# Performance work log

Measured on AMD Instinct MI355X. Metric: run time of the kernel, lower is better.

The kernel has to match this reference:

```python
import jax, jax.numpy as jnp
import numpy as np

MIN_EXPERTS = 1
MAX_EXPERTS = 8
TEMPERATURE = 1.0


def setup_inputs() -> dict:
    key = jax.random.key(0)
    ks = jax.random.split(key, 7)
    B, S, H, E = 8, 4096, 1024, 64
    Hh = H // 2
    return {
        "hidden_states": jax.random.normal(ks[0], (B, S, H), dtype=jnp.float32),
        "W_router": jax.random.normal(ks[1], (E, H), dtype=jnp.float32) * 0.02,
        "b_router": jax.random.normal(ks[2], (E,), dtype=jnp.float32) * 0.02,
        "W1": jax.random.normal(ks[3], (Hh, H), dtype=jnp.float32) * 0.02,
        "b1": jax.random.normal(ks[4], (Hh,), dtype=jnp.float32) * 0.02,
        "W2": jax.random.normal(ks[5], (1, Hh), dtype=jnp.float32) * 0.02,
        "b2": jax.random.normal(ks[6], (1,), dtype=jnp.float32) * 0.02,
    }


def reference(hidden_states, W_router, b_router, W1, b1, W2, b2):
    B, S, H = hidden_states.shape
    flat = hidden_states.reshape(-1, H)                     # [N, H]

    # router logits
    router_logits = (flat @ W_router.T + b_router) / TEMPERATURE  # [N, E]

    # confidence net: Linear -> ReLU -> Linear -> Sigmoid
    h = jax.nn.relu(flat @ W1.T + b1)                       # [N, H/2]
    confidence = jax.nn.sigmoid(h @ W2.T + b2).squeeze(-1)  # [N]

    # dynamic k per token (torch.round = half-to-even, same as jnp.round)
    dk = MIN_EXPERTS + (MAX_EXPERTS - MIN_EXPERTS) * (1.0 - confidence)
    dk = jnp.clip(jnp.round(dk), MIN_EXPERTS, MAX_EXPERTS).astype(jnp.int32)  # [N]

    routing_probs = jax.nn.softmax(router_logits, axis=-1)  # [N, E]

    # single top-k pass replaces per-iteration sort; mask slots >= dynamic_k
    top_vals, top_idx = jax.lax.top_k(routing_probs, MAX_EXPERTS)  # [N, max_k]
    slot = jnp.arange(MAX_EXPERTS, dtype=jnp.int32)[None, :]       # [1, max_k]
    active = slot < dk[:, None]                                    # [N, max_k]
    sel_w = jnp.where(active, top_vals, 0.0)
    sel_i = jnp.where(active, top_idx, 0).astype(jnp.int64)

    sel_w = sel_w.reshape(B, S, MAX_EXPERTS)
    sel_i = sel_i.reshape(B, S, MAX_EXPERTS)
    return sel_w, sel_i, confidence, router_logits
```

## Files before the change

### kernel.cpp

```cpp
#include <hip/hip_runtime.h>
#include <hip/hip_bf16.h>
#include <math.h>

#define N_TOK 32768
#define HDIM 1024
#define HH 512
#define NOUT 576
#define BM 256
#define BN 64
#define BK 32
#define THREADS 256
#define KC 384

#define OFF_SELW 0
#define OFF_SELI 262144
#define OFF_CONF 524288
#define OFF_LOG  557056

__device__ float  g_Bmat[HDIM * NOUT];
__device__ double g_partial[N_TOK * 8];

__global__ __launch_bounds__(256) void k_build(const float* __restrict__ W1,
                                               const float* __restrict__ Wr) {
  int idx = blockIdx.x * 256 + threadIdx.x;
  int k = idx / NOUT;
  int j = idx - k * NOUT;
  float v = (j < HH) ? W1[(size_t)j * HDIM + k] : Wr[(size_t)(j - HH) * HDIM + k];
  g_Bmat[idx] = v;
}

__global__ __launch_bounds__(THREADS, 2) void k_gemm(const float* __restrict__ A,
                                                     const float* __restrict__ b1,
                                                     const float* __restrict__ W2,
                                                     const float* __restrict__ b_router,
                                                     float* __restrict__ out_logits) {
  __shared__ float As[BK][BM];
  __shared__ float Bs[BK][BN];

  int bid = blockIdx.x;
  int xcd = bid & 7;
  int s   = bid >> 3;
  int j   = s % 9;
  int t   = xcd + 8 * (s / 9);

  const int tid = threadIdx.x;
  const int tx  = tid & 7;
  const int ty  = tid >> 3;
  const int m0  = t * BM;
  const int n0  = j * BN;

  float acc[8][8];
  float carry[8][8];
  #pragma unroll
  for (int i = 0; i < 8; ++i)
    #pragma unroll
    for (int c = 0; c < 8; ++c) { acc[i][c] = 0.f; carry[i][c] = 0.f; }

  const float* Ag = A + (size_t)(m0 + tid) * HDIM;

  for (int k0 = 0; k0 < HDIM; k0 += BK) {
    if (k0 == KC || k0 == 2 * KC) {
      #pragma unroll
      for (int i = 0; i < 8; ++i)
        #pragma unroll
        for (int c = 0; c < 8; ++c) {
          carry[i][c] = carry[i][c] + acc[i][c];
          acc[i][c] = 0.f;
        }
    }

    float4 av[8];
    #pragma unroll
    for (int c = 0; c < 8; ++c)
      av[c] = *(const float4*)(Ag + k0 + c * 4);
    float4 bv[2];
    #pragma unroll
    for (int c = 0; c < 2; ++c) {
      int idx = tid + c * 256;
      int kr  = idx >> 4;
      int ch  = idx & 15;
      bv[c] = *(const float4*)&g_Bmat[(size_t)(k0 + kr) * NOUT + n0 + ch * 4];
    }
    __syncthreads();
    #pragma unroll
    for (int c = 0; c < 8; ++c) {
      int kb = c * 4;
      As[kb + 0][tid] = av[c].x;
      As[kb + 1][tid] = av[c].y;
      As[kb + 2][tid] = av[c].z;
      As[kb + 3][tid] = av[c].w;
    }
    #pragma unroll
    for (int c = 0; c < 2; ++c) {
      int idx = tid + c * 256;
      int kr  = idx >> 4;
      int ch  = idx & 15;
      *(float4*)&Bs[kr][ch * 4] = bv[c];
    }
    __syncthreads();

    #pragma unroll 4
    for (int kk = 0; kk < BK; ++kk) {
      float4 a03 = *(const float4*)&As[kk][ty * 8 + 0];
      float4 a47 = *(const float4*)&As[kk][ty * 8 + 4];
      float4 b03 = *(const float4*)&Bs[kk][tx * 8 + 0];
      float4 b47 = *(const float4*)&Bs[kk][tx * 8 + 4];
      float a[8] = {a03.x, a03.y, a03.z, a03.w, a47.x, a47.y, a47.z, a47.w};
      float b[8] = {b03.x, b03.y, b03.z, b03.w, b47.x, b47.y, b47.z, b47.w};
      #pragma unroll
      for (int i = 0; i < 8; ++i)
        #pragma unroll
        for (int c = 0; c < 8; ++c)
          acc[i][c] = fmaf(a[i], b[c], acc[i][c]);
    }
  }

  #pragma unroll
  for (int i = 0; i < 8; ++i)
    #pragma unroll
    for (int c = 0; c < 8; ++c) carry[i][c] = carry[i][c] + acc[i][c];

  if (j < 8) {
    double w2v[8];
    float  b1v[8];
    #pragma unroll
    for (int c = 0; c < 8; ++c) {
      w2v[c] = (double)W2[n0 + tx * 8 + c];
      b1v[c] = b1[n0 + tx * 8 + c];
    }
    #pragma unroll
    for (int i = 0; i < 8; ++i) {
      double sacc = 0.0;
      #pragma unroll
      for (int c = 0; c < 8; ++c) {
        float h = fmaxf(carry[i][c] + b1v[c], 0.f);
        sacc = fma((double)h, w2v[c], sacc);
      }
      sacc += __shfl_xor(sacc, 1, 64);
      sacc += __shfl_xor(sacc, 2, 64);
      sacc += __shfl_xor(sacc, 4, 64);
      if (tx == 0) g_partial[(size_t)(m0 + ty * 8 + i) * 8 + j] = sacc;
    }
  } else {
    float brv[8];
    #pragma unroll
    for (int c = 0; c < 8; ++c) brv[c] = b_router[tx * 8 + c];
    #pragma unroll
    for (int i = 0; i < 8; ++i) {
      int row = m0 + ty * 8 + i;
      float o[8];
      #pragma unroll
      for (int c = 0; c < 8; ++c) o[c] = carry[i][c] + brv[c];
      float* dst = out_logits + (size_t)row * 64 + tx * 8;
      *(float4*)dst       = make_float4(o[0], o[1], o[2], o[3]);
      *(float4*)(dst + 4) = make_float4(o[4], o[5], o[6], o[7]);
    }
  }
}

__global__ __launch_bounds__(256, 2) void k_post(const float* __restrict__ b2,
                                                 float* __restrict__ d_out) {
  int tk = blockIdx.x * 256 + threadIdx.x;

  double ca = (double)b2[0];
  #pragma unroll
  for (int jj = 0; jj < 8; ++jj) ca += g_partial[(size_t)tk * 8 + jj];
  double conf = 1.0 / (1.0 + exp(-ca));
  double dkf  = 1.0 + 7.0 * (1.0 - conf);
  double dkr  = rint(dkf);
  int dk = (int)fmin(fmax(dkr, 1.0), 8.0);

  const float* logits = d_out + OFF_LOG + (size_t)tk * 64;
  float x[64];
  #pragma unroll
  for (int e4 = 0; e4 < 16; ++e4)
    *(float4*)&x[e4 * 4] = *(const float4*)&logits[e4 * 4];

  float mx = x[0];
  #pragma unroll
  for (int e = 1; e < 64; ++e) mx = fmaxf(mx, x[e]);

  #pragma unroll
  for (int e = 0; e < 64; ++e) x[e] = expf(x[e] - mx);

  float r[8];
  #pragma unroll
  for (int q = 0; q < 8; ++q) r[q] = x[q];
  #pragma unroll
  for (int b = 1; b < 8; ++b)
    #pragma unroll
    for (int q = 0; q < 8; ++q) r[q] += x[b * 8 + q];
  float ssum = ((r[0] + r[1]) + (r[2] + r[3])) + ((r[4] + r[5]) + (r[6] + r[7]));

  #pragma unroll
  for (int e = 0; e < 64; ++e) x[e] = x[e] / ssum;

  float* sel_w = d_out + OFF_SELW + (size_t)tk * 8;
  float* sel_i = d_out + OFF_SELI + (size_t)tk * 8;
  unsigned long long used = 0ull;
  #pragma unroll
  for (int slot = 0; slot < 8; ++slot) {
    float best = -1.f;
    int   bi   = 0;
    #pragma unroll
    for (int e = 0; e < 64; ++e) {
      bool ok = (((used >> e) & 1ull) == 0ull) && (x[e] > best);
      best = ok ? x[e] : best;
      bi   = ok ? e    : bi;
    }
    used |= (1ull << bi);
    bool active = slot < dk;
    sel_w[slot] = active ? best : 0.f;
    sel_i[slot] = active ? (float)bi : 0.f;
  }
  d_out[OFF_CONF + tk] = (float)conf;
}

extern "C" void kernel_launch(void* const* d_in, const int* in_sizes, int n_in,
                              void* d_out, int out_size, void* d_ws, size_t ws_size,
                              hipStream_t stream) {
  const float* hidden   = (const float*)d_in[0];
  const float* W_router = (const float*)d_in[1];
  const float* b_router = (const float*)d_in[2];
  const float* W1       = (const float*)d_in[3];
  const float* b1       = (const float*)d_in[4];
  const float* W2       = (const float*)d_in[5];
  const float* b2       = (const float*)d_in[6];
  float* out = (float*)d_out;

  k_build<<<(HDIM * NOUT) / 256, 256, 0, stream>>>(W1, W_router);
  k_gemm<<<(N_TOK / BM) * 9, THREADS, 0, stream>>>(hidden, b1, W2, b_router,
                                                   out + OFF_LOG);
  k_post<<<N_TOK / 256, 256, 0, stream>>>(b2, out);
}
```

Before: 699.0 us.

## Replace LDS-tiled GEMM with per-thread row dot products over 16-column tiles

The shared-memory tiled 8x8 register-blocked GEMM is replaced by a scheme where each thread owns one token row and computes 16 output columns. A comes straight from global memory as float4, and B rows are uniform across the wave, so they become broadcast/scalar loads. This removes the LDS staging and barriers and raises occupancy. In exchange, each thread issues uncoalesced strided loads of its own A row, and A is re-read 36 times instead of 9. The confidence partial sums grow from 8 to 32 per token.

```diff
diff --git a/kernel.cpp b/kernel.cpp
--- a/kernel.cpp
+++ b/kernel.cpp
@@ -6,19 +6,17 @@
 #define HDIM 1024
 #define HH 512
 #define NOUT 576
-#define BM 256
-#define BN 64
-#define BK 32
+#define CT 16
+#define NCT 36
 #define THREADS 256
-#define KC 384
 
 #define OFF_SELW 0
 #define OFF_SELI 262144
 #define OFF_CONF 524288
 #define OFF_LOG  557056
 
-__device__ float  g_Bmat[HDIM * NOUT];
-__device__ double g_partial[N_TOK * 8];
+__device__ __attribute__((aligned(256))) float g_Bmat[HDIM * NOUT];
+__device__ double g_partial[N_TOK * 32];
 
 __global__ __launch_bounds__(256) void k_build(const float* __restrict__ W1,
                                                const float* __restrict__ Wr) {
@@ -29,132 +27,64 @@
   g_Bmat[idx] = v;
 }
 
-__global__ __launch_bounds__(THREADS, 2) void k_gemm(const float* __restrict__ A,
+__global__ __launch_bounds__(THREADS, 8) void k_gemm(const float* __restrict__ A,
                                                      const float* __restrict__ b1,
                                                      const float* __restrict__ W2,
                                                      const float* __restrict__ b_router,
                                                      float* __restrict__ out_logits) {
-  __shared__ float As[BK][BM];
-  __shared__ float Bs[BK][BN];
-
   int bid = blockIdx.x;
   int xcd = bid & 7;
   int s   = bid >> 3;
-  int j   = s % 9;
-  int t   = xcd + 8 * (s / 9);
+  int ct  = s % NCT;
+  int tg  = xcd + 8 * (s / NCT);
 
-  const int tid = threadIdx.x;
-  const int tx  = tid & 7;
-  const int ty  = tid >> 3;
-  const int m0  = t * BM;
-  const int n0  = j * BN;
+  const int m  = tg * 256 + threadIdx.x;
+  const int j0 = ct * CT;
 
-  float acc[8][8];
-  float carry[8][8];
+  const float* __restrict__ Ag = A + (size_t)m * HDIM;
+  const float* __restrict__ Bg = g_Bmat + j0;
+
+  float acc[CT], carry[CT];
   #pragma unroll
-  for (int i = 0; i < 8; ++i)
-    #pragma unroll
-    for (int c = 0; c < 8; ++c) { acc[i][c] = 0.f; carry[i][c] = 0.f; }
+  for (int c = 0; c < CT; ++c) { acc[c] = 0.f; carry[c] = 0.f; }
 
-  const float* Ag = A + (size_t)(m0 + tid) * HDIM;
-
-  for (int k0 = 0; k0 < HDIM; k0 += BK) {
-    if (k0 == KC || k0 == 2 * KC) {
+  const int kb[4] = {0, 384, 768, 1024};
+  #pragma unroll
+  for (int p = 0; p < 3; ++p) {
+    for (int k0 = kb[p]; k0 < kb[p + 1]; k0 += 4) {
+      float4 av = *(const float4*)(Ag + k0);
+      const float a4[4] = {av.x, av.y, av.z, av.w};
       #pragma unroll
-      for (int i = 0; i < 8; ++i)
+      for (int kk = 0; kk < 4; ++kk) {
+        const float* __restrict__ brow = Bg + (size_t)(k0 + kk) * NOUT;
+        float a = a4[kk];
         #pragma unroll
-        for (int c = 0; c < 8; ++c) {
-          carry[i][c] = carry[i][c] + acc[i][c];
-          acc[i][c] = 0.f;
-        }
-    }
-
-    float4 av[8];
-    #pragma unroll
-    for (int c = 0; c < 8; ++c)
-      av[c] = *(const float4*)(Ag + k0 + c * 4);
-    float4 bv[2];
-    #pragma unroll
-    for (int c = 0; c < 2; ++c) {
-      int idx = tid + c * 256;
-      int kr  = idx >> 4;
-      int ch  = idx & 15;
-      bv[c] = *(const float4*)&g_Bmat[(size_t)(k0 + kr) * NOUT + n0 + ch * 4];
-    }
-    __syncthreads();
-    #pragma unroll
-    for (int c = 0; c < 8; ++c) {
-      int kb = c * 4;
-      As[kb + 0][tid] = av[c].x;
-      As[kb + 1][tid] = av[c].y;
-      As[kb + 2][tid] = av[c].z;
-      As[kb + 3][tid] = av[c].w;
+        for (int c = 0; c < CT; ++c)
+          acc[c] = fmaf(a, brow[c], acc[c]);
+      }
     }
     #pragma unroll
-    for (int c = 0; c < 2; ++c) {
-      int idx = tid + c * 256;
-      int kr  = idx >> 4;
-      int ch  = idx & 15;
-      *(float4*)&Bs[kr][ch * 4] = bv[c];
-    }
-    __syncthreads();
-
-    #pragma unroll 4
-    for (int kk = 0; kk < BK; ++kk) {
-      float4 a03 = *(const float4*)&As[kk][ty * 8 + 0];
-      float4 a47 = *(const float4*)&As[kk][ty * 8 + 4];
-      float4 b03 = *(const float4*)&Bs[kk][tx * 8 + 0];
-      float4 b47 = *(const float4*)&Bs[kk][tx * 8 + 4];
-      float a[8] = {a03.x, a03.y, a03.z, a03.w, a47.x, a47.y, a47.z, a47.w};
-      float b[8] = {b03.x, b03.y, b03.z, b03.w, b47.x, b47.y, b47.z, b47.w};
-      #pragma unroll
-      for (int i = 0; i < 8; ++i)
-        #pragma unroll
-        for (int c = 0; c < 8; ++c)
-          acc[i][c] = fmaf(a[i], b[c], acc[i][c]);
-    }
+    for (int c = 0; c < CT; ++c) { carry[c] = carry[c] + acc[c]; acc[c] = 0.f; }
   }
 
-  #pragma unroll
-  for (int i = 0; i < 8; ++i)
+  if (ct < 32) {
+    double sacc = 0.0;
     #pragma unroll
-    for (int c = 0; c < 8; ++c) carry[i][c] = carry[i][c] + acc[i][c];
-
-  if (j < 8) {
-    double w2v[8];
-    float  b1v[8];
+    for (int c = 0; c < CT; ++c) {
+      float h = fmaxf(carry[c] + b1[j0 + c], 0.f);
+      sacc = fma((double)h, (double)W2[j0 + c], sacc);
+    }
+    g_partial[(size_t)m * 32 + ct] = sacc;
+  } else {
+    int jr = (ct - 32) * CT;
+    float o[CT];
     #pragma unroll
-    for (int c = 0; c < 8; ++c) {
-      w2v[c] = (double)W2[n0 + tx * 8 + c];
-      b1v[c] = b1[n0 + tx * 8 + c];
-    }
+    for (int c = 0; c < CT; ++c) o[c] = carry[c] + b_router[jr + c];
+    float* dst = out_logits + (size_t)m * 64 + jr;
     #pragma unroll
-    for (int i = 0; i < 8; ++i) {
-      double sacc = 0.0;
-      #pragma unroll
-      for (int c = 0; c < 8; ++c) {
-        float h = fmaxf(carry[i][c] + b1v[c], 0.f);
-        sacc = fma((double)h, w2v[c], sacc);
-      }
-      sacc += __shfl_xor(sacc, 1, 64);
-      sacc += __shfl_xor(sacc, 2, 64);
-      sacc += __shfl_xor(sacc, 4, 64);
-      if (tx == 0) g_partial[(size_t)(m0 + ty * 8 + i) * 8 + j] = sacc;
-    }
-  } else {
-    float brv[8];
-    #pragma unroll
-    for (int c = 0; c < 8; ++c) brv[c] = b_router[tx * 8 + c];
-    #pragma unroll
-    for (int i = 0; i < 8; ++i) {
-      int row = m0 + ty * 8 + i;
-      float o[8];
-      #pragma unroll
-      for (int c = 0; c < 8; ++c) o[c] = carry[i][c] + brv[c];
-      float* dst = out_logits + (size_t)row * 64 + tx * 8;
-      *(float4*)dst       = make_float4(o[0], o[1], o[2], o[3]);
-      *(float4*)(dst + 4) = make_float4(o[4], o[5], o[6], o[7]);
-    }
+    for (int c4 = 0; c4 < 4; ++c4)
+      *(float4*)(dst + c4 * 4) =
+          make_float4(o[c4 * 4], o[c4 * 4 + 1], o[c4 * 4 + 2], o[c4 * 4 + 3]);
   }
 }
 
@@ -164,7 +94,7 @@
 
   double ca = (double)b2[0];
   #pragma unroll
-  for (int jj = 0; jj < 8; ++jj) ca += g_partial[(size_t)tk * 8 + jj];
+  for (int jj = 0; jj < 32; ++jj) ca += g_partial[(size_t)tk * 32 + jj];
   double conf = 1.0 / (1.0 + exp(-ca));
   double dkf  = 1.0 + 7.0 * (1.0 - conf);
   double dkr  = rint(dkf);
@@ -229,7 +159,7 @@
   float* out = (float*)d_out;
 
   k_build<<<(HDIM * NOUT) / 256, 256, 0, stream>>>(W1, W_router);
-  k_gemm<<<(N_TOK / BM) * 9, THREADS, 0, stream>>>(hidden, b1, W2, b_router,
-                                                   out + OFF_LOG);
+  k_gemm<<<(N_TOK / 256) * NCT, THREADS, 0, stream>>>(hidden, b1, W2, b_router,
+                                                      out + OFF_LOG);
   k_post<<<N_TOK / 256, 256, 0, stream>>>(b2, out);
 }
```

New measurement: 1.387 ms. 98.4% more time.
